# Optimization experiments

Measured on AMD Instinct MI355X. Metric: run time of the kernel, lower is better.

Reference implementation:

```python
import jax, jax.numpy as jnp
import numpy as np
import math

IN_DIM = 4096
OUT_DIM = 4096
NR_CORES = 3
RANK = 16
D = 16  # in_core_size == out_core_size == 16, 16**3 == 4096


def _core_std():
    t = 1.0 / math.sqrt(0.5 * (IN_DIM + OUT_DIM))
    return (t * math.sqrt(RANK) ** (1 - NR_CORES)) ** (1.0 / NR_CORES)


def setup_inputs() -> dict:
    key = jax.random.key(0)
    kx, k0, k1, k2, kb = jax.random.split(key, 5)
    sigma = _core_std()
    x = jax.random.normal(kx, (4, 2048, IN_DIM), dtype=jnp.float32)
    core0 = sigma * jax.random.normal(k0, (1, D, D, RANK), dtype=jnp.float32)
    core1 = sigma * jax.random.normal(k1, (RANK, D, D, RANK), dtype=jnp.float32)
    core2 = sigma * jax.random.normal(k2, (RANK, D, D, 1), dtype=jnp.float32)
    # kaiming_uniform on (1, out_dim): bound = sqrt(6 / fan_in), fan_in = out_dim
    bound = math.sqrt(6.0 / OUT_DIM)
    bias = jax.random.uniform(kb, (OUT_DIM,), dtype=jnp.float32, minval=-bound, maxval=bound)
    return {"x": x, "core0": core0, "core1": core1, "core2": core2, "bias": bias}


def reference(x, core0, core1, core2, bias):
    # Materialize dense weight G [out_dim, in_dim] from 3 TT cores, as in TT.to_matrix()
    G = jnp.einsum('ainb,bjmc,ckod->aijknmod', core0, core1, core2)
    G = G.reshape(OUT_DIM, IN_DIM)
    shape = x.shape
    x2 = x.reshape(-1, shape[-1])          # [BS, in_dim]
    out = x2 @ G.T + bias                  # addmm(bias, x, G.T)
    return out.reshape(*shape[:-1], OUT_DIM)
```

## Files before the change

### kernel.cpp

```cpp
#include <hip/hip_runtime.h>


typedef short bf16x8 __attribute__((ext_vector_type(8)));
typedef float f32x4 __attribute__((ext_vector_type(4)));

__device__ __forceinline__ unsigned short f2bf_rne(float f) {
  union { float f; unsigned int i; } v;
  v.f = f;
  unsigned int r = v.i + 0x7FFFu + ((v.i >> 16) & 1u);
  return (unsigned short)(r >> 16);
}

__device__ __forceinline__ unsigned int pk2bf_rne(float lo, float hi) {
  return (unsigned int)f2bf_rne(lo) | ((unsigned int)f2bf_rne(hi) << 16);
}

__device__ __forceinline__ unsigned int pk2bf_trunc(float lo, float hi) {
  union { float f; unsigned int u; } a, b;
  a.f = lo; b.f = hi;
  return (b.u & 0xFFFF0000u) | (a.u >> 16);
}

__device__ __forceinline__ void gl2lds16(const void* g, void* l) {
  __builtin_amdgcn_global_load_lds(
      (__attribute__((address_space(1))) void*)g,
      (__attribute__((address_space(3))) void*)l, 16u, 0, 0u);
}

__global__ __launch_bounds__(256) void cvt_x(const float* __restrict__ x,
                                             unsigned short* __restrict__ xb) {
  const size_t t = (size_t)blockIdx.x * 256 + threadIdx.x;
  const float4 a0 = *(const float4*)(x + t * 8);
  const float4 a1 = *(const float4*)(x + t * 8 + 4);
  uint4 w = {pk2bf_rne(a0.x, a0.y), pk2bf_rne(a0.z, a0.w),
             pk2bf_rne(a1.x, a1.y), pk2bf_rne(a1.z, a1.w)};
  *(uint4*)(xb + t * 8) = w;
}

__global__ __launch_bounds__(256, 1) void build_g(
    const float* __restrict__ core0,
    const float* __restrict__ core1,
    const float* __restrict__ core2,
    unsigned short* __restrict__ G) {
  __shared__ float c0s[256];
  __shared__ float c1s[16 * 320];
  __shared__ float c2s[4096];
  __shared__ float Hs[256 * 20];
  const int t = threadIdx.x;
  const int blk = blockIdx.x;
  const int i = blk >> 4, j = blk & 15;

  c0s[t] = core0[i * 256 + t];
  {
    const int m = t >> 4, c = t & 15;
#pragma unroll
    for (int b = 0; b < 16; b++)
      c1s[b * 320 + m * 20 + c] = core1[b * 4096 + j * 256 + t];
  }
#pragma unroll
  for (int q = 0; q < 16; q++) c2s[q * 256 + t] = core2[q * 256 + t];
  __syncthreads();

  {
    const int n = t >> 4, m = t & 15;
    f32x4 hv0 = {0.f, 0.f, 0.f, 0.f}, hv1 = hv0, hv2 = hv0, hv3 = hv0;
#pragma unroll
    for (int b = 0; b < 16; b++) {
      const float a = c0s[n * 16 + b];
      const f32x4* p = (const f32x4*)&c1s[b * 320 + m * 20];
      hv0 += a * p[0];
      hv1 += a * p[1];
      hv2 += a * p[2];
      hv3 += a * p[3];
    }
    f32x4* hp = (f32x4*)&Hs[t * 20];
    hp[0] = hv0; hp[1] = hv1; hp[2] = hv2; hp[3] = hv3;
  }
  __syncthreads();

  const int w = t >> 6, l = t & 63;
  f32x4 hr[4][4];
#pragma unroll
  for (int q = 0; q < 4; q++) {
    const f32x4* hp = (const f32x4*)&Hs[(l + 64 * q) * 20];
#pragma unroll
    for (int d = 0; d < 4; d++) hr[q][d] = hp[d];
  }

#pragma unroll
  for (int kk = 0; kk < 4; kk++) {
    const int k = w * 4 + kk;
    f32x4 acc[4][4];
    const f32x4 zero = {0.f, 0.f, 0.f, 0.f};
#pragma unroll
    for (int q = 0; q < 4; q++)
#pragma unroll
      for (int d = 0; d < 4; d++) acc[q][d] = zero;

#pragma unroll
    for (int c = 0; c < 16; c++) {
      const f32x4* cp = (const f32x4*)&c2s[c * 256 + k * 16];
      const f32x4 cv0 = cp[0], cv1 = cp[1], cv2 = cp[2], cv3 = cp[3];
#pragma unroll
      for (int q = 0; q < 4; q++) {
        const float hqc = hr[q][c >> 2][c & 3];
        acc[q][0] += hqc * cv0;
        acc[q][1] += hqc * cv1;
        acc[q][2] += hqc * cv2;
        acc[q][3] += hqc * cv3;
      }
    }

    const size_t rowbase = (size_t)(blk * 16 + k) * 4096;
#pragma unroll
    for (int q = 0; q < 4; q++) {
      unsigned int u[8];
#pragma unroll
      for (int d = 0; d < 8; d++)
        u[d] = pk2bf_rne(acc[q][d >> 1][(d & 1) * 2],
                         acc[q][d >> 1][(d & 1) * 2 + 1]);
      uint4* gp = (uint4*)&G[rowbase + (size_t)(l + 64 * q) * 16];
      uint4 s0 = {u[0], u[1], u[2], u[3]};
      uint4 s1 = {u[4], u[5], u[6], u[7]};
      gp[0] = s0;
      gp[1] = s1;
    }
  }
}

constexpr int Mdim = 8192, Ndim = 4096, Kdim = 4096;

__global__ __launch_bounds__(512, 2) void gemm_8ph(
    const unsigned short* __restrict__ A,
    const unsigned short* __restrict__ Bt,
    const float* __restrict__ bias,
    float* __restrict__ C) {
  __shared__ __align__(16) unsigned short sA[2][2][8192];
  __shared__ __align__(16) unsigned short sB[2][2][8192];

  const int tid = threadIdx.x, lane = tid & 63, wave = tid >> 6;
  const int wm = wave >> 2, wn = wave & 3;

  const int bid = (int)blockIdx.x;
  const int swz = (bid & 7) * 64 + (bid >> 3);
  const int bm0 = (swz >> 4) * 256, bn0 = (swz & 15) * 256;

  const int srow = 8 * wave + (lane >> 3);
  const int scol = ((lane & 7) ^ (lane >> 3)) * 8;
  const unsigned short* Ag = A + (size_t)(bm0 + srow) * Kdim + scol;
  const unsigned short* Bg = Bt + (size_t)(bn0 + srow) * Kdim + scol;
  unsigned short* Asl = &sA[0][0][0] + wave * 512 + lane * 8;
  unsigned short* Bsl = &sB[0][0][0] + wave * 512 + lane * 8;

#define STG_A(slot, half, kt)                                                  \
  do {                                                                         \
    gl2lds16(Ag + (size_t)(128 * (half)) * Kdim + (kt) * 64,                   \
             Asl + (slot) * 16384 + (half) * 8192);                            \
    gl2lds16(Ag + (size_t)(128 * (half) + 64) * Kdim + (kt) * 64,              \
             Asl + (slot) * 16384 + (half) * 8192 + 4096);                     \
  } while (0)
#define STG_B(slot, half, kt)                                                  \
  do {                                                                         \
    gl2lds16(Bg + (size_t)(128 * (half)) * Kdim + (kt) * 64,                   \
             Bsl + (slot) * 16384 + (half) * 8192);                            \
    gl2lds16(Bg + (size_t)(128 * (half) + 64) * Kdim + (kt) * 64,              \
             Bsl + (slot) * 16384 + (half) * 8192 + 4096);                     \
  } while (0)

  const int r15 = lane & 15, quad = lane >> 4;
  const int cs0 = ((quad) ^ (lane & 7)) * 8;
  const int cs1 = ((4 + quad) ^ (lane & 7)) * 8;
  const unsigned short* Ard = &sA[0][wm][0] + r15 * 64;
  const unsigned short* Brd = &sB[0][wn >> 1][0] + ((wn & 1) * 64 + r15) * 64;

  bf16x8 afr[4][2];
  bf16x8 bfr[4][2];
  f32x4 acc[8][4];
  const f32x4 zero = {0.f, 0.f, 0.f, 0.f};
#pragma unroll
  for (int a = 0; a < 8; a++)
#pragma unroll
    for (int b = 0; b < 4; b++) acc[a][b] = zero;

#define LDA(slot, a)                                                           \
  do {                                                                         \
    _Pragma("unroll") for (int m = 0; m < 4; ++m) {                            \
      afr[m][0] = *(const bf16x8*)(Ard + (slot) * 16384 +                      \
                                   ((a) * 64 + m * 16) * 64 + cs0);            \
      afr[m][1] = *(const bf16x8*)(Ard + (slot) * 16384 +                      \
                                   ((a) * 64 + m * 16) * 64 + cs1);            \
    }                                                                          \
  } while (0)
#define LDB2(slot, nlo)                                                        \
  do {                                                                         \
    _Pragma("unroll") for (int n = 0; n < 2; ++n) {                            \
      bfr[(nlo) + n][0] = *(const bf16x8*)(Brd + (slot) * 16384 +              \
                                           ((nlo) + n) * 16 * 64 + cs0);       \
      bfr[(nlo) + n][1] = *(const bf16x8*)(Brd + (slot) * 16384 +              \
                                           ((nlo) + n) * 16 * 64 + cs1);       \
    }                                                                          \
  } while (0)
#define MMQ(a, bh)                                                             \
  do {                                                                         \
    _Pragma("unroll") for (int m = 0; m < 4; ++m)                              \
        _Pragma("unroll") for (int n = 0; n < 2; ++n) {                        \
      acc[(a)*4 + m][(bh)*2 + n] = __builtin_amdgcn_mfma_f32_16x16x32_bf16(    \
          afr[m][0], bfr[(bh)*2 + n][0], acc[(a)*4 + m][(bh)*2 + n], 0, 0, 0); \
      acc[(a)*4 + m][(bh)*2 + n] = __builtin_amdgcn_mfma_f32_16x16x32_bf16(    \
          afr[m][1], bfr[(bh)*2 + n][1], acc[(a)*4 + m][(bh)*2 + n], 0, 0, 0); \
    }                                                                          \
  } while (0)

#define BAR asm volatile("s_barrier" ::: "memory")
#define WLG0 asm volatile("s_waitcnt lgkmcnt(0)" ::: "memory")
#define WLG8 asm volatile("s_waitcnt lgkmcnt(8)" ::: "memory")
#define WVM0 asm volatile("s_waitcnt vmcnt(0)" ::: "memory")
#define WVM4 asm volatile("s_waitcnt vmcnt(4)" ::: "memory")
#define SBAR0 __builtin_amdgcn_sched_barrier(0)
#define PRIO1 __builtin_amdgcn_s_setprio(1)
#define PRIO0 __builtin_amdgcn_s_setprio(0)

  STG_A(0, 0, 0); STG_A(0, 1, 0); STG_B(0, 0, 0); STG_B(0, 1, 0);
  SBAR0;
  WVM0;
  SBAR0;
  STG_B(1, 0, 1); STG_B(1, 1, 1);
  SBAR0;
  BAR;

#pragma unroll 1
  for (int i = 0; i < Kdim / 128; ++i) {
    const int t1 = 2 * i + 1;
    const int u0 = (2 * i + 2) & 63;
    const int u1 = (2 * i + 3) & 63;
    LDA(0, 0); LDB2(0, 0);
    STG_A(1, 0, t1);
    WLG8; BAR; WLG0; PRIO1; MMQ(0, 0); PRIO0; BAR;
    LDB2(0, 2);
    STG_A(1, 1, t1);
    BAR; WLG0; PRIO1; MMQ(0, 1); PRIO0; BAR;
    LDA(0, 1);
    STG_B(0, 0, u0);
    BAR; WLG0; PRIO1; MMQ(1, 1); PRIO0; BAR;
    STG_B(0, 1, u0);
    BAR; PRIO1; MMQ(1, 0); PRIO0; WVM4; BAR;
    LDA(1, 0); LDB2(1, 0);
    STG_A(0, 0, u0);
    WLG8; BAR; WLG0; PRIO1; MMQ(0, 0); PRIO0; BAR;
    LDB2(1, 2);
    STG_A(0, 1, u0);
    BAR; WLG0; PRIO1; MMQ(0, 1); PRIO0; BAR;
    LDA(1, 1);
    STG_B(1, 0, u1);
    BAR; WLG0; PRIO1; MMQ(1, 1); PRIO0; BAR;
    STG_B(1, 1, u1);
    BAR; PRIO1; MMQ(1, 0); PRIO0; WVM4; BAR;
  }

  WVM0;

#pragma unroll
  for (int nf = 0; nf < 4; ++nf) {
    const int n = bn0 + wn * 64 + nf * 16 + r15;
    const float bv = bias[n];
#pragma unroll
    for (int am = 0; am < 8; ++am) {
      const int mb = bm0 + wm * 128 + am * 16 + quad * 4;
#pragma unroll
      for (int r = 0; r < 4; ++r)
        C[(size_t)(mb + r) * Ndim + n] = acc[am][nf][r] + bv;
    }
  }
#undef STG_A
#undef STG_B
#undef LDA
#undef LDB2
#undef MMQ
#undef BAR
#undef WLG0
#undef WLG8
#undef WVM0
#undef WVM4
#undef SBAR0
#undef PRIO1
#undef PRIO0
}

__global__ __launch_bounds__(256, 3) void gemm_pack(
    const float* __restrict__ A, const unsigned short* __restrict__ Bt,
    const float* __restrict__ bias, float* __restrict__ C) {
  __shared__ __align__(16) unsigned short lA[128 * 32];
  __shared__ __align__(16) unsigned short lB[128 * 32];
  const int tid = threadIdx.x, lane = tid & 63, wave = tid >> 6;
  const int bm0 = blockIdx.y * 128, bn0 = blockIdx.x * 128;
  const int wm = wave >> 1, wn = wave & 1;
  const int srow = lane >> 2, scol = (lane & 3) * 8;
  const unsigned short* Bg = Bt + (size_t)(bn0 + wave * 32 + srow) * Kdim + scol;
  unsigned short* lBp = &lB[wave * 32 * 32 + lane * 8];
  const int arow = wave * 16 + (lane >> 2);
  const int acol = (lane & 3) * 8;
  const float* Ag0 = A + (size_t)(bm0 + arow) * Kdim + acol;
  const float* Ag1 = Ag0 + (size_t)64 * Kdim;
  uint4* lAw0 = (uint4*)&lA[tid * 8];
  uint4* lAw1 = (uint4*)&lA[2048 + tid * 8];

  f32x4 acc[4][4];
  const f32x4 zero = {0.f, 0.f, 0.f, 0.f};
#pragma unroll
  for (int a = 0; a < 4; a++)
#pragma unroll
    for (int b = 0; b < 4; b++) acc[a][b] = zero;
  const int row = lane & 15, quad = lane >> 4;

  for (int k0 = 0; k0 < Kdim; k0 += 32) {
    __syncthreads();
    gl2lds16(Bg + k0, lBp);
    gl2lds16(Bg + k0 + 16 * Kdim, lBp + 16 * 32);
    float4 a0 = *(const float4*)(Ag0 + k0);
    float4 a1 = *(const float4*)(Ag0 + k0 + 4);
    float4 a2 = *(const float4*)(Ag1 + k0);
    float4 a3 = *(const float4*)(Ag1 + k0 + 4);
    uint4 w0 = {pk2bf_trunc(a0.x, a0.y), pk2bf_trunc(a0.z, a0.w),
                pk2bf_trunc(a1.x, a1.y), pk2bf_trunc(a1.z, a1.w)};
    uint4 w1 = {pk2bf_trunc(a2.x, a2.y), pk2bf_trunc(a2.z, a2.w),
                pk2bf_trunc(a3.x, a3.y), pk2bf_trunc(a3.z, a3.w)};
    *lAw0 = w0;
    *lAw1 = w1;
    __syncthreads();

    bf16x8 af[4], bfv[4];
#pragma unroll
    for (int mi = 0; mi < 4; mi++)
      af[mi] = *(const bf16x8*)&lA[(wm * 64 + mi * 16 + row) * 32 + quad * 8];
#pragma unroll
    for (int ni = 0; ni < 4; ni++)
      bfv[ni] = *(const bf16x8*)&lB[(wn * 64 + ni * 16 + row) * 32 + quad * 8];
#pragma unroll
    for (int mi = 0; mi < 4; mi++)
#pragma unroll
      for (int ni = 0; ni < 4; ni++)
        acc[mi][ni] = __builtin_amdgcn_mfma_f32_16x16x32_bf16(
            af[mi], bfv[ni], acc[mi][ni], 0, 0, 0);
  }
#pragma unroll
  for (int ni = 0; ni < 4; ni++) {
    const int n = bn0 + wn * 64 + ni * 16 + row;
    const float bv = bias[n];
#pragma unroll
    for (int mi = 0; mi < 4; mi++) {
      const int mbase = bm0 + wm * 64 + mi * 16 + quad * 4;
#pragma unroll
      for (int r = 0; r < 4; r++)
        C[(size_t)(mbase + r) * Ndim + n] = acc[mi][ni][r] + bv;
    }
  }
}

extern "C" void kernel_launch(void* const* d_in, const int* in_sizes, int n_in,
                              void* d_out, int out_size, void* d_ws,
                              size_t ws_size, hipStream_t stream) {
  const float* x = (const float*)d_in[0];
  const float* core0 = (const float*)d_in[1];
  const float* core1 = (const float*)d_in[2];
  const float* core2 = (const float*)d_in[3];
  const float* bias = (const float*)d_in[4];
  float* out = (float*)d_out;

  unsigned short* G = (unsigned short*)d_ws;
  const size_t G_BYTES = (size_t)4096 * 4096 * 2;
  const size_t X_BYTES = (size_t)Mdim * Kdim * 2;

  build_g<<<256, 256, 0, stream>>>(core0, core1, core2, G);

  if (ws_size >= G_BYTES + X_BYTES) {
    unsigned short* Xb = (unsigned short*)((char*)d_ws + G_BYTES);
    cvt_x<<<(Mdim * Kdim) / (256 * 8), 256, 0, stream>>>(x, Xb);
    gemm_8ph<<<(Mdim / 256) * (Ndim / 256), 512, 0, stream>>>(Xb, G, bias, out);
  } else {
    dim3 grid(Ndim / 128, Mdim / 128);
    gemm_pack<<<grid, 256, 0, stream>>>(x, G, bias, out);
  }
}
```

Baseline: 467.8 us.

## Split build_g into 4096 blocks, one output row each

The dense-weight builder now launches one block per output row (i,j,k) instead of one per (i,j) pair. Each block recomputes the core0×core1 intermediate and contracts it with a single 16-slice of core2. This cuts shared memory and register use and spreads the work across far more blocks to raise occupancy on the many CUs. In exchange the H intermediate is computed 16 times redundantly and core0/core1 are reloaded per block.

Result: no change. 469.9 us (+0.5%).

```diff
diff --git a/kernel.cpp b/kernel.cpp
--- a/kernel.cpp
+++ b/kernel.cpp
@@ -37,18 +37,17 @@
   *(uint4*)(xb + t * 8) = w;
 }
 
-__global__ __launch_bounds__(256, 1) void build_g(
+__global__ __launch_bounds__(256) void build_g(
     const float* __restrict__ core0,
     const float* __restrict__ core1,
     const float* __restrict__ core2,
     unsigned short* __restrict__ G) {
   __shared__ float c0s[256];
   __shared__ float c1s[16 * 320];
-  __shared__ float c2s[4096];
-  __shared__ float Hs[256 * 20];
+  __shared__ float c2s[256];
   const int t = threadIdx.x;
-  const int blk = blockIdx.x;
-  const int i = blk >> 4, j = blk & 15;
+  const int bid = blockIdx.x;
+  const int i = bid >> 8, j = (bid >> 4) & 15, k = bid & 15;
 
   c0s[t] = core0[i * 256 + t];
   {
@@ -57,75 +56,46 @@
     for (int b = 0; b < 16; b++)
       c1s[b * 320 + m * 20 + c] = core1[b * 4096 + j * 256 + t];
   }
-#pragma unroll
-  for (int q = 0; q < 16; q++) c2s[q * 256 + t] = core2[q * 256 + t];
+  c2s[t] = core2[(t >> 4) * 256 + k * 16 + (t & 15)];
   __syncthreads();
 
-  {
-    const int n = t >> 4, m = t & 15;
-    f32x4 hv0 = {0.f, 0.f, 0.f, 0.f}, hv1 = hv0, hv2 = hv0, hv3 = hv0;
-#pragma unroll
-    for (int b = 0; b < 16; b++) {
-      const float a = c0s[n * 16 + b];
-      const f32x4* p = (const f32x4*)&c1s[b * 320 + m * 20];
-      hv0 += a * p[0];
-      hv1 += a * p[1];
-      hv2 += a * p[2];
-      hv3 += a * p[3];
-    }
-    f32x4* hp = (f32x4*)&Hs[t * 20];
-    hp[0] = hv0; hp[1] = hv1; hp[2] = hv2; hp[3] = hv3;
-  }
-  __syncthreads();
-
-  const int w = t >> 6, l = t & 63;
-  f32x4 hr[4][4];
-#pragma unroll
-  for (int q = 0; q < 4; q++) {
-    const f32x4* hp = (const f32x4*)&Hs[(l + 64 * q) * 20];
-#pragma unroll
-    for (int d = 0; d < 4; d++) hr[q][d] = hp[d];
-  }
-
-#pragma unroll
-  for (int kk = 0; kk < 4; kk++) {
-    const int k = w * 4 + kk;
-    f32x4 acc[4][4];
-    const f32x4 zero = {0.f, 0.f, 0.f, 0.f};
-#pragma unroll
-    for (int q = 0; q < 4; q++)
-#pragma unroll
-      for (int d = 0; d < 4; d++) acc[q][d] = zero;
-
-#pragma unroll
-    for (int c = 0; c < 16; c++) {
-      const f32x4* cp = (const f32x4*)&c2s[c * 256 + k * 16];
-      const f32x4 cv0 = cp[0], cv1 = cp[1], cv2 = cp[2], cv3 = cp[3];
-#pragma unroll
-      for (int q = 0; q < 4; q++) {
-        const float hqc = hr[q][c >> 2][c & 3];
-        acc[q][0] += hqc * cv0;
-        acc[q][1] += hqc * cv1;
-        acc[q][2] += hqc * cv2;
-        acc[q][3] += hqc * cv3;
-      }
-    }
-
-    const size_t rowbase = (size_t)(blk * 16 + k) * 4096;
-#pragma unroll
-    for (int q = 0; q < 4; q++) {
-      unsigned int u[8];
-#pragma unroll
-      for (int d = 0; d < 8; d++)
-        u[d] = pk2bf_rne(acc[q][d >> 1][(d & 1) * 2],
-                         acc[q][d >> 1][(d & 1) * 2 + 1]);
-      uint4* gp = (uint4*)&G[rowbase + (size_t)(l + 64 * q) * 16];
-      uint4 s0 = {u[0], u[1], u[2], u[3]};
-      uint4 s1 = {u[4], u[5], u[6], u[7]};
-      gp[0] = s0;
-      gp[1] = s1;
-    }
-  }
+  const int n = t >> 4, m = t & 15;
+
+  f32x4 h0 = {0.f, 0.f, 0.f, 0.f}, h1 = h0, h2 = h0, h3 = h0;
+#pragma unroll
+  for (int b = 0; b < 16; b++) {
+    const float a = c0s[n * 16 + b];
+    const f32x4* p = (const f32x4*)&c1s[b * 320 + m * 20];
+    h0 += a * p[0];
+    h1 += a * p[1];
+    h2 += a * p[2];
+    h3 += a * p[3];
+  }
+  f32x4 h4[4] = {h0, h1, h2, h3};
+
+  f32x4 o4[4];
+  const f32x4 zero = {0.f, 0.f, 0.f, 0.f};
+#pragma unroll
+  for (int d = 0; d < 4; d++) o4[d] = zero;
+#pragma unroll
+  for (int c = 0; c < 16; c++) {
+    const float hv = h4[c >> 2][c & 3];
+    const f32x4* cp = (const f32x4*)&c2s[c * 16];
+    o4[0] += hv * cp[0];
+    o4[1] += hv * cp[1];
+    o4[2] += hv * cp[2];
+    o4[3] += hv * cp[3];
+  }
+
+  unsigned int u[8];
+#pragma unroll
+  for (int d = 0; d < 8; d++)
+    u[d] = pk2bf_rne(o4[d >> 1][(d & 1) * 2], o4[d >> 1][(d & 1) * 2 + 1]);
+  uint4* gp = (uint4*)&G[(size_t)bid * 4096 + t * 16];
+  uint4 s0 = {u[0], u[1], u[2], u[3]};
+  uint4 s1 = {u[4], u[5], u[6], u[7]};
+  gp[0] = s0;
+  gp[1] = s1;
 }
 
 constexpr int Mdim = 8192, Ndim = 4096, Kdim = 4096;
@@ -370,7 +340,7 @@
   const size_t G_BYTES = (size_t)4096 * 4096 * 2;
   const size_t X_BYTES = (size_t)Mdim * Kdim * 2;
 
-  build_g<<<256, 256, 0, stream>>>(core0, core1, core2, G);
+  build_g<<<4096, 256, 0, stream>>>(core0, core1, core2, G);
 
   if (ws_size >= G_BYTES + X_BYTES) {
     unsigned short* Xb = (unsigned short*)((char*)d_ws + G_BYTES);
```
